# Kernel tuning notes

Measured on AMD Instinct MI355X. Metric: run time of the kernel, lower is better.

The kernel has to match this reference:

```python
import jax, jax.numpy as jnp
import numpy as np

B, T, C = 4, 2048, 768
H, KVH, D = 6, 6, 128
HALF = D // 2


def setup_inputs() -> dict:
    key = jax.random.key(0)
    ks = jax.random.split(key, 5)
    x = jax.random.normal(ks[0], (B, T, C), dtype=jnp.float32)
    # true rotary frequencies
    inv_freq = 1.0 / (10000.0 ** (jnp.arange(HALF, dtype=jnp.float32) / HALF))
    ang = jnp.arange(T, dtype=jnp.float32)[:, None] * inv_freq[None, :]  # [T, HALF]
    cos, sin = jnp.cos(ang), jnp.sin(ang)
    s = 0.02
    wq = jax.random.normal(ks[1], (H * D, C), dtype=jnp.float32) * s
    wk = jax.random.normal(ks[2], (KVH * D, C), dtype=jnp.float32) * s
    wv = jax.random.normal(ks[3], (KVH * D, C), dtype=jnp.float32) * s
    wproj = jax.random.normal(ks[4], (C, C), dtype=jnp.float32) * s
    return {"x": x, "cos": cos, "sin": sin, "wq": wq, "wk": wk, "wv": wv, "wproj": wproj}


def _norm(t, eps=1e-6):
    # torch: (x - mean) / (std + eps), std unbiased (ddof=1)
    mean = jnp.mean(t, axis=-1, keepdims=True)
    var = jnp.sum((t - mean) ** 2, axis=-1, keepdims=True) / (t.shape[-1] - 1)
    return (t - mean) / (jnp.sqrt(var) + eps)


def _rope(t, cos, sin):
    # t: [B, T, heads, D]; cos/sin: [T, HALF]
    x1, x2 = t[..., :HALF], t[..., HALF:]
    c = cos[None, :, None, :]
    s = sin[None, :, None, :]
    return jnp.concatenate([x1 * c + x2 * s, -x1 * s + x2 * c], axis=-1)


def reference(x, cos, sin, wq, wk, wv, wproj):
    q = jnp.einsum('btc,oc->bto', x, wq).reshape(B, T, H, D)
    k = jnp.einsum('btc,oc->bto', x, wk).reshape(B, T, KVH, D)
    v = jnp.einsum('btc,oc->bto', x, wv).reshape(B, T, KVH, D)
    q = _norm(_rope(q, cos, sin))
    k = _norm(_rope(k, cos, sin))
    # -> [B, heads, T, D]
    q = q.transpose(0, 2, 1, 3)
    k = k.transpose(0, 2, 1, 3)
    v = v.transpose(0, 2, 1, 3)
    # nrep = H // KVH == 1, repeat_kv is a no-op here
    scale = 1.0 / jnp.sqrt(jnp.float32(D))
    scores = jnp.einsum('bhtd,bhsd->bhts', q, k) * scale  # [B,H,T,T]
    causal = jnp.tril(jnp.ones((T, T), dtype=bool))
    scores = jnp.where(causal[None, None], scores, jnp.float32(-1e30))
    attn = jax.nn.softmax(scores, axis=-1)
    y = jnp.einsum('bhts,bhsd->bhtd', attn, v)
    y = y.transpose(0, 2, 1, 3).reshape(B, T, H * D)
    return jnp.einsum('bto,co->btc', y, wproj)
```

## Files before the change

### kernel.cpp

```cpp
#include <hip/hip_runtime.h>

#define BB 4
#define TT 2048
#define CC 768
#define HH 6
#define DD 128
#define BT (BB * TT)
#define HALF 64
#define QKSCALE 0.12753785627919282f

typedef __bf16 v8bf __attribute__((ext_vector_type(8)));
typedef float f32x4 __attribute__((ext_vector_type(4)));

__device__ __forceinline__ unsigned short f2b(float f) {
  union { float f; unsigned u; } v; v.f = f;
  unsigned r = v.u + 0x7FFFu + ((v.u >> 16) & 1u);
  return (unsigned short)(r >> 16);
}

__device__ __forceinline__ void load_lds16(const void* g, void* l) {
  __builtin_amdgcn_global_load_lds(
      (const __attribute__((address_space(1))) unsigned int*)g,
      (__attribute__((address_space(3))) unsigned int*)(unsigned int)(unsigned long long)(l),
      16, 0, 0);
}

__global__ __launch_bounds__(256) void cvt_f2b_kernel(const float* __restrict__ src,
                                                      unsigned short* __restrict__ dst,
                                                      int n4) {
  int i = blockIdx.x * 256 + threadIdx.x;
  if (i >= n4) return;
  float4 f = ((const float4*)src)[i];
  ushort4 o;
  o.x = f2b(f.x); o.y = f2b(f.y); o.z = f2b(f.z); o.w = f2b(f.w);
  ((ushort4*)dst)[i] = o;
}

__global__ __launch_bounds__(256) void cvt_w4_kernel(const float* __restrict__ w0,
                                                     const float* __restrict__ w1,
                                                     const float* __restrict__ w2,
                                                     const float* __restrict__ w3,
                                                     unsigned short* __restrict__ dst) {
  int bsel = blockIdx.x / 576;
  int i = (blockIdx.x % 576) * 256 + threadIdx.x;
  const float* src = bsel == 0 ? w0 : bsel == 1 ? w1 : bsel == 2 ? w2 : w3;
  float4 f = ((const float4*)src)[i];
  ushort4 o;
  o.x = f2b(f.x); o.y = f2b(f.y); o.z = f2b(f.z); o.w = f2b(f.w);
  ((ushort4*)(dst + bsel * 589824))[i] = o;
}

__global__ __launch_bounds__(256) void gemm_qkv(const unsigned short* __restrict__ A,
                                                const unsigned short* __restrict__ Wall,
                                                float* __restrict__ qout,
                                                float* __restrict__ kout,
                                                unsigned short* __restrict__ vt) {
  __shared__ __align__(16) unsigned short As[2][512 * 8];
  __shared__ __align__(16) unsigned short Bs[2][512 * 8];
  const int m0 = blockIdx.x * 128;
  const int wsel = blockIdx.y / HH, h = blockIdx.y % HH;
  const unsigned short* W = Wall + (size_t)wsel * 589824 + (size_t)h * 128 * CC;
  const int tid = threadIdx.x;
  const int wave = tid >> 6, lane = tid & 63;
  const int fr = lane & 15, quad = lane >> 4;
  const int wm = (wave & 1) * 64, wn = (wave >> 1) * 64;

  f32x4 acc[4][4];
#pragma unroll
  for (int i = 0; i < 4; i++)
#pragma unroll
    for (int j = 0; j < 4; j++) acc[i][j] = (f32x4){0.f, 0.f, 0.f, 0.f};

  auto stage = [&](int kk, int buf) {
#pragma unroll
    for (int it = 0; it < 2; it++) {
      int base_slot = wave * 128 + it * 64;
      int sigma = base_slot + lane;
      int r = sigma >> 2, g = (sigma & 3) ^ ((r >> 1) & 3);
      load_lds16(A + (size_t)(m0 + r) * CC + kk + g * 8, &As[buf][base_slot * 8]);
      load_lds16(W + (size_t)r * CC + kk + g * 8, &Bs[buf][base_slot * 8]);
    }
  };

  stage(0, 0);
  __syncthreads();
  for (int step = 0; step < CC / 32; step++) {
    int buf = step & 1;
    if (step + 1 < CC / 32) stage((step + 1) * 32, buf ^ 1);
    v8bf af[4], bfr[4];
#pragma unroll
    for (int i = 0; i < 4; i++) {
      int ra = wm + i * 16 + fr;
      af[i] = *(const v8bf*)&As[buf][(4 * ra + (quad ^ ((ra >> 1) & 3))) * 8];
      int rb = wn + i * 16 + fr;
      bfr[i] = *(const v8bf*)&Bs[buf][(4 * rb + (quad ^ ((rb >> 1) & 3))) * 8];
    }
#pragma unroll
    for (int i = 0; i < 4; i++)
#pragma unroll
      for (int j = 0; j < 4; j++)
        acc[i][j] = __builtin_amdgcn_mfma_f32_16x16x32_bf16(af[i], bfr[j], acc[i][j], 0, 0, 0);
    __syncthreads();
  }

  if (wsel < 2) {
    float* out = wsel ? kout : qout;
    const int orow = m0 + wm + quad * 4;
#pragma unroll
    for (int i = 0; i < 4; i++)
#pragma unroll
      for (int j = 0; j < 4; j++) {
        int oc = h * 128 + wn + j * 16 + fr;
#pragma unroll
        for (int r = 0; r < 4; r++)
          out[(size_t)(orow + i * 16 + r) * CC + oc] = acc[i][j][r];
      }
  } else {
#pragma unroll
    for (int i = 0; i < 4; i++) {
      int rr0 = m0 + wm + i * 16 + quad * 4;
      int b = rr0 >> 11, t0 = rr0 & 2047;
      int bh = b * HH + h;
#pragma unroll
      for (int j = 0; j < 4; j++) {
        int d = wn + j * 16 + fr;
        ushort4 u = { f2b(acc[i][j][0]), f2b(acc[i][j][1]),
                      f2b(acc[i][j][2]), f2b(acc[i][j][3]) };
        *(ushort4*)&vt[((size_t)bh * DD + d) * TT + t0] = u;
      }
    }
  }
}

__global__ __launch_bounds__(256) void gemm_w64(const unsigned short* __restrict__ A,
                                                const unsigned short* __restrict__ W,
                                                float* __restrict__ C) {
  __shared__ __align__(16) unsigned short As[2][256 * 8];
  __shared__ __align__(16) unsigned short Bs[2][512 * 8];
  const int m0 = blockIdx.x * 64, n0 = blockIdx.y * 128;
  const int tid = threadIdx.x;
  const int wave = tid >> 6, lane = tid & 63;
  const int fr = lane & 15, quad = lane >> 4;
  const int wm = (wave & 1) * 32, wn = (wave >> 1) * 64;

  f32x4 acc[2][4];
#pragma unroll
  for (int i = 0; i < 2; i++)
#pragma unroll
    for (int j = 0; j < 4; j++) acc[i][j] = (f32x4){0.f, 0.f, 0.f, 0.f};

  auto stage = [&](int kk, int buf) {
    {
      int base_slot = wave * 64;
      int sigma = base_slot + lane;
      int r = sigma >> 2, g = (sigma & 3) ^ ((r >> 1) & 3);
      load_lds16(A + (size_t)(m0 + r) * CC + kk + g * 8, &As[buf][base_slot * 8]);
    }
#pragma unroll
    for (int it = 0; it < 2; it++) {
      int base_slot = wave * 128 + it * 64;
      int sigma = base_slot + lane;
      int r = sigma >> 2, g = (sigma & 3) ^ ((r >> 1) & 3);
      load_lds16(W + (size_t)(n0 + r) * CC + kk + g * 8, &Bs[buf][base_slot * 8]);
    }
  };

  stage(0, 0);
  __syncthreads();
  for (int step = 0; step < CC / 32; step++) {
    int buf = step & 1;
    if (step + 1 < CC / 32) stage((step + 1) * 32, buf ^ 1);
    v8bf af[2], bfr[4];
#pragma unroll
    for (int i = 0; i < 2; i++) {
      int ra = wm + i * 16 + fr;
      af[i] = *(const v8bf*)&As[buf][(4 * ra + (quad ^ ((ra >> 1) & 3))) * 8];
    }
#pragma unroll
    for (int j = 0; j < 4; j++) {
      int rb = wn + j * 16 + fr;
      bfr[j] = *(const v8bf*)&Bs[buf][(4 * rb + (quad ^ ((rb >> 1) & 3))) * 8];
    }
#pragma unroll
    for (int i = 0; i < 2; i++)
#pragma unroll
      for (int j = 0; j < 4; j++)
        acc[i][j] = __builtin_amdgcn_mfma_f32_16x16x32_bf16(af[i], bfr[j], acc[i][j], 0, 0, 0);
    __syncthreads();
  }

  const int orow = m0 + wm + quad * 4;
#pragma unroll
  for (int i = 0; i < 2; i++)
#pragma unroll
    for (int j = 0; j < 4; j++) {
      int oc = n0 + wn + j * 16 + fr;
#pragma unroll
      for (int r = 0; r < 4; r++)
        C[(size_t)(orow + i * 16 + r) * CC + oc] = acc[i][j][r];
    }
}

__global__ __launch_bounds__(256) void rope_norm_kernel(const float* __restrict__ src,
                                                        unsigned short* __restrict__ dst,
                                                        const float* __restrict__ cosb,
                                                        const float* __restrict__ sinb) {
  int idx = blockIdx.x * 4 + (threadIdx.x >> 6);
  int lane = threadIdx.x & 63;
  int h = idx % HH;
  int bt = idx / HH;
  int tpos = bt & (TT - 1);
  int b = bt >> 11;
  size_t base = (size_t)bt * CC + h * DD;

  float x1 = src[base + lane];
  float x2 = src[base + HALF + lane];
  float c = cosb[tpos * HALF + lane];
  float s = sinb[tpos * HALF + lane];
  float o1 = x1 * c + x2 * s;
  float o2 = x2 * c - x1 * s;

  float sum = o1 + o2;
#pragma unroll
  for (int off = 32; off; off >>= 1) sum += __shfl_xor(sum, off);
  float mean = sum * (1.f / 128.f);
  float d1 = o1 - mean, d2 = o2 - mean;
  float vs = d1 * d1 + d2 * d2;
#pragma unroll
  for (int off = 32; off; off >>= 1) vs += __shfl_xor(vs, off);
  float inv = 1.f / (sqrtf(vs * (1.f / 127.f)) + 1e-6f);

  size_t obase = (((size_t)b * HH + h) * TT + tpos) * DD;
  dst[obase + lane] = f2b(d1 * inv);
  dst[obase + HALF + lane] = f2b(d2 * inv);
}

__global__ __launch_bounds__(128) void attn_mfma(const unsigned short* __restrict__ qtb,
                                                 const unsigned short* __restrict__ ktb,
                                                 const unsigned short* __restrict__ vtb,
                                                 float* __restrict__ Opart,
                                                 float* __restrict__ lpart) {
  __shared__ __align__(16) unsigned short Ks[2][512 * 8];
  __shared__ __align__(16) unsigned short Vts[2][512 * 8];
  __shared__ __align__(16) unsigned short Ps[2][32][40];

  const int u = blockIdx.x;
  const int qt = (TT / 64 - 1) - u / 48;
  const int r48 = u % 48;
  const int chunk = r48 / 24;
  const int bh = r48 % 24;
  const int tid = threadIdx.x;
  const int wave = tid >> 6, lane = tid & 63;
  const int fr = lane & 15, quad = lane >> 4;

  const size_t head_base = (size_t)bh * TT * DD;
  const int m0 = qt * 64 + wave * 32;
  const int jt0 = chunk ? (qt + 1) : 0;
  const int niter = qt + 1;

  v8bf qf[2][4];
#pragma unroll
  for (int qs = 0; qs < 2; qs++)
#pragma unroll
    for (int kb = 0; kb < 4; kb++)
      qf[qs][kb] = *(const v8bf*)(qtb + head_base +
                                  (size_t)(m0 + qs * 16 + fr) * DD + kb * 32 + quad * 8);

  f32x4 oacc[2][8];
#pragma unroll
  for (int qs = 0; qs < 2; qs++)
#pragma unroll
    for (int i = 0; i < 8; i++) oacc[qs][i] = (f32x4){0.f, 0.f, 0.f, 0.f};
  float lsum[2] = {0.f, 0.f};

  auto stage = [&](int jt, int buf) {
    const unsigned short* kbase = ktb + head_base + (size_t)(jt * 32) * DD;
    const unsigned short* vbase = vtb + head_base + jt * 32;
#pragma unroll
    for (int it = 0; it < 4; it++) {
      int base_slot = wave * 256 + it * 64;
      int sigma = base_slot + lane;
      int s = sigma >> 4, gk = (sigma & 15) ^ (s & 7);
      load_lds16(kbase + (size_t)s * DD + gk * 8, &Ks[buf][base_slot * 8]);
      int d = sigma >> 2, gv = (sigma & 3) ^ ((d >> 1) & 3);
      load_lds16(vbase + (size_t)d * TT + gv * 8, &Vts[buf][base_slot * 8]);
    }
  };

  stage(jt0, 0);
  __syncthreads();

  for (int it = 0; it < niter; it++) {
    const int jt = jt0 + it;
    const int buf = it & 1;
    if (it + 1 < niter) stage(jt + 1, buf ^ 1);

    if (jt * 32 <= m0 + 31) {
      const int j0 = jt * 32;
      f32x4 st[2][2];
#pragma unroll
      for (int qs = 0; qs < 2; qs++) { st[qs][0] = (f32x4){0,0,0,0}; st[qs][1] = (f32x4){0,0,0,0}; }
#pragma unroll
      for (int kb = 0; kb < 4; kb++) {
        int g = 4 * kb + quad;
        v8bf a0 = *(const v8bf*)&Ks[buf][(16 * fr + (g ^ (fr & 7))) * 8];
        v8bf a1 = *(const v8bf*)&Ks[buf][(16 * (fr + 16) + (g ^ (fr & 7))) * 8];
        st[0][0] = __builtin_amdgcn_mfma_f32_16x16x32_bf16(a0, qf[0][kb], st[0][0], 0, 0, 0);
        st[0][1] = __builtin_amdgcn_mfma_f32_16x16x32_bf16(a1, qf[0][kb], st[0][1], 0, 0, 0);
        st[1][0] = __builtin_amdgcn_mfma_f32_16x16x32_bf16(a0, qf[1][kb], st[1][0], 0, 0, 0);
        st[1][1] = __builtin_amdgcn_mfma_f32_16x16x32_bf16(a1, qf[1][kb], st[1][1], 0, 0, 0);
      }

#pragma unroll
      for (int qs = 0; qs < 2; qs++) {
        const int qrow = m0 + qs * 16 + fr;
        float p[8]; float ls = 0.f;
#pragma unroll
        for (int r = 0; r < 4; r++) {
          int c0 = j0 + quad * 4 + r;
          p[r]     = (c0      <= qrow) ? exp2f(st[qs][0][r] * QKSCALE) : 0.f;
          p[4 + r] = (c0 + 16 <= qrow) ? exp2f(st[qs][1][r] * QKSCALE) : 0.f;
          ls += p[r] + p[4 + r];
        }
        lsum[qs] += ls;
        ushort4 w0 = { f2b(p[0]), f2b(p[1]), f2b(p[2]), f2b(p[3]) };
        ushort4 w1 = { f2b(p[4]), f2b(p[5]), f2b(p[6]), f2b(p[7]) };
        *(ushort4*)&Ps[wave][qs * 16 + fr][quad * 4] = w0;
        *(ushort4*)&Ps[wave][qs * 16 + fr][16 + quad * 4] = w1;
      }

      v8bf pa0 = *(const v8bf*)&Ps[wave][fr][quad * 8];
      v8bf pa1 = *(const v8bf*)&Ps[wave][16 + fr][quad * 8];
#pragma unroll
      for (int nt2 = 0; nt2 < 8; nt2++) {
        int d = nt2 * 16 + fr;
        v8bf vb = *(const v8bf*)&Vts[buf][(4 * d + (quad ^ ((d >> 1) & 3))) * 8];
        oacc[0][nt2] = __builtin_amdgcn_mfma_f32_16x16x32_bf16(pa0, vb, oacc[0][nt2], 0, 0, 0);
        oacc[1][nt2] = __builtin_amdgcn_mfma_f32_16x16x32_bf16(pa1, vb, oacc[1][nt2], 0, 0, 0);
      }
    }
    __syncthreads();
  }

  float* Oc = Opart + (size_t)chunk * (BB * HH * TT * DD) + head_base;
#pragma unroll
  for (int qs = 0; qs < 2; qs++) {
    float l = lsum[qs];
    l += __shfl_xor(l, 16);
    l += __shfl_xor(l, 32);
    if (quad == 0)
      lpart[chunk * (BB * HH * TT) + bh * TT + m0 + qs * 16 + fr] = l;
#pragma unroll
    for (int nt2 = 0; nt2 < 8; nt2++)
#pragma unroll
      for (int r = 0; r < 4; r++)
        Oc[(size_t)(m0 + qs * 16 + quad * 4 + r) * DD + nt2 * 16 + fr] = oacc[qs][nt2][r];
  }
}

__global__ __launch_bounds__(256) void combine_kernel(const float* __restrict__ Opart,
                                                      const float* __restrict__ lpart,
                                                      unsigned short* __restrict__ yb) {
  int idx = blockIdx.x * 256 + threadIdx.x;
  int row = idx >> 5;
  int dg = (idx & 31) * 4;
  float4 o0 = *(const float4*)&Opart[(size_t)row * DD + dg];
  float4 o1 = *(const float4*)&Opart[(size_t)(BB * HH * TT) * DD + (size_t)row * DD + dg];
  float linv = 1.f / (lpart[row] + lpart[BB * HH * TT + row]);
  int bh = row >> 11, t = row & 2047;
  int b = bh / HH, h = bh % HH;
  ushort4 u = { f2b((o0.x + o1.x) * linv), f2b((o0.y + o1.y) * linv),
                f2b((o0.z + o1.z) * linv), f2b((o0.w + o1.w) * linv) };
  *(ushort4*)&yb[((size_t)(b * TT + t)) * CC + h * DD + dg] = u;
}

extern "C" void kernel_launch(void* const* d_in, const int* in_sizes, int n_in,
                              void* d_out, int out_size, void* d_ws, size_t ws_size,
                              hipStream_t stream) {
  const float* x     = (const float*)d_in[0];
  const float* cosb  = (const float*)d_in[1];
  const float* sinb  = (const float*)d_in[2];
  const float* wq    = (const float*)d_in[3];
  const float* wk    = (const float*)d_in[4];
  const float* wv    = (const float*)d_in[5];
  const float* wproj = (const float*)d_in[6];
  float* out = (float*)d_out;

  char* w = (char*)d_ws;
  float* q     = (float*)(w);
  float* kk    = (float*)(w + 25165824);
  float* Opart = (float*)(w);
  unsigned short* yb  = (unsigned short*)(w + 50331648);
  unsigned short* v_t = (unsigned short*)(w + 62914560);
  unsigned short* q_t = (unsigned short*)(w + 75497472);
  unsigned short* k_t = (unsigned short*)(w + 88080384);
  unsigned short* xb  = (unsigned short*)(w + 100663296);
  float* lpart        = (float*)(w + 100663296);
  unsigned short* wb  = (unsigned short*)(w + 113246208);

  const int nx4 = BT * CC / 4;

  cvt_f2b_kernel<<<nx4 / 256, 256, 0, stream>>>(x, xb, nx4);
  cvt_w4_kernel<<<2304, 256, 0, stream>>>(wq, wk, wv, wproj, wb);

  gemm_qkv<<<dim3(BT / 128, 3 * HH), 256, 0, stream>>>(xb, wb, q, kk, v_t);

  int nvec = BT * HH;
  rope_norm_kernel<<<nvec / 4, 256, 0, stream>>>(q, q_t, cosb, sinb);
  rope_norm_kernel<<<nvec / 4, 256, 0, stream>>>(kk, k_t, cosb, sinb);

  attn_mfma<<<1536, 128, 0, stream>>>(q_t, k_t, v_t, Opart, lpart);
  combine_kernel<<<6144, 256, 0, stream>>>(Opart, lpart, yb);

  gemm_w64<<<dim3(BT / 64, CC / 128), 256, 0, stream>>>(yb, wb + 3 * 589824, out);
}
```

Measured before the change: 245.4 us.

## Store Q/K as bf16 head-major, split attention into balanced KV chunks

The QKV GEMM now writes Q and K directly as bf16 in head-major layout, and rope/norm runs in place with the softmax scale folded into Q. This removes the fp32 round trip and the transposing write. The attention kernel is restructured into 4 waves of 16 query rows each, with a variable number of 16-tile KV chunks per query tile to balance causal work across 1920 blocks. It also skips the mask on full tiles, computes row sums with an MFMA against ones, and stores bf16 partial outputs. The combine kernel then sums a variable number of bf16 partials, which adds precision risk from bf16 partial accumulation and from the unbounded exp2 without a running max.

Result: no change. 246.8 us (+0.6%).

```diff
diff --git a/kernel.cpp b/kernel.cpp
--- a/kernel.cpp
+++ b/kernel.cpp
@@ -7,15 +7,30 @@
 #define DD 128
 #define BT (BB * TT)
 #define HALF 64
+#define NBH (BB * HH)
 #define QKSCALE 0.12753785627919282f
 
 typedef __bf16 v8bf __attribute__((ext_vector_type(8)));
 typedef float f32x4 __attribute__((ext_vector_type(4)));
+
+#if __has_builtin(__builtin_amdgcn_exp2f)
+#define EXP2(x) __builtin_amdgcn_exp2f(x)
+#else
+#define EXP2(x) exp2f(x)
+#endif
 
 __device__ __forceinline__ unsigned short f2b(float f) {
   union { float f; unsigned u; } v; v.f = f;
   unsigned r = v.u + 0x7FFFu + ((v.u >> 16) & 1u);
   return (unsigned short)(r >> 16);
+}
+__device__ __forceinline__ float b2f(unsigned short u) {
+  union { unsigned u; float f; } v; v.u = (unsigned)u << 16;
+  return v.f;
+}
+__device__ __forceinline__ unsigned pk2(float f0, float f1) {
+  union { float f; unsigned u; } a, b; a.f = f1; b.f = f0;
+  return __builtin_amdgcn_perm(a.u, b.u, 0x07060302u);
 }
 
 __device__ __forceinline__ void load_lds16(const void* g, void* l) {
@@ -52,8 +67,8 @@
 
 __global__ __launch_bounds__(256) void gemm_qkv(const unsigned short* __restrict__ A,
                                                 const unsigned short* __restrict__ Wall,
-                                                float* __restrict__ qout,
-                                                float* __restrict__ kout,
+                                                unsigned short* __restrict__ qb,
+                                                unsigned short* __restrict__ kb,
                                                 unsigned short* __restrict__ vt) {
   __shared__ __align__(16) unsigned short As[2][512 * 8];
   __shared__ __align__(16) unsigned short Bs[2][512 * 8];
@@ -104,17 +119,20 @@
   }
 
   if (wsel < 2) {
-    float* out = wsel ? kout : qout;
-    const int orow = m0 + wm + quad * 4;
-#pragma unroll
-    for (int i = 0; i < 4; i++)
+    unsigned short* dst = wsel ? kb : qb;
+#pragma unroll
+    for (int i = 0; i < 4; i++) {
+      int rr0 = m0 + wm + i * 16 + quad * 4;
+      int b = rr0 >> 11, t0 = rr0 & 2047;
+      size_t base = ((size_t)(b * HH + h) * TT + t0) * DD;
 #pragma unroll
       for (int j = 0; j < 4; j++) {
-        int oc = h * 128 + wn + j * 16 + fr;
+        int d = wn + j * 16 + fr;
 #pragma unroll
         for (int r = 0; r < 4; r++)
-          out[(size_t)(orow + i * 16 + r) * CC + oc] = acc[i][j][r];
+          dst[base + (size_t)r * DD + d] = f2b(acc[i][j][r]);
       }
+    }
   } else {
 #pragma unroll
     for (int i = 0; i < 4; i++) {
@@ -201,20 +219,17 @@
     }
 }
 
-__global__ __launch_bounds__(256) void rope_norm_kernel(const float* __restrict__ src,
-                                                        unsigned short* __restrict__ dst,
+__global__ __launch_bounds__(256) void rope_norm_kernel(unsigned short* __restrict__ qk,
                                                         const float* __restrict__ cosb,
-                                                        const float* __restrict__ sinb) {
+                                                        const float* __restrict__ sinb,
+                                                        float scale) {
   int idx = blockIdx.x * 4 + (threadIdx.x >> 6);
   int lane = threadIdx.x & 63;
-  int h = idx % HH;
-  int bt = idx / HH;
-  int tpos = bt & (TT - 1);
-  int b = bt >> 11;
-  size_t base = (size_t)bt * CC + h * DD;
-
-  float x1 = src[base + lane];
-  float x2 = src[base + HALF + lane];
+  int tpos = idx & (TT - 1);
+  size_t base = (size_t)idx * DD;
+
+  float x1 = b2f(qk[base + lane]);
+  float x2 = b2f(qk[base + HALF + lane]);
   float c = cosb[tpos * HALF + lane];
   float s = sinb[tpos * HALF + lane];
   float o1 = x1 * c + x2 * s;
@@ -228,57 +243,58 @@
   float vs = d1 * d1 + d2 * d2;
 #pragma unroll
   for (int off = 32; off; off >>= 1) vs += __shfl_xor(vs, off);
-  float inv = 1.f / (sqrtf(vs * (1.f / 127.f)) + 1e-6f);
-
-  size_t obase = (((size_t)b * HH + h) * TT + tpos) * DD;
-  dst[obase + lane] = f2b(d1 * inv);
-  dst[obase + HALF + lane] = f2b(d2 * inv);
-}
-
-__global__ __launch_bounds__(128) void attn_mfma(const unsigned short* __restrict__ qtb,
+  float inv = scale / (sqrtf(vs * (1.f / 127.f)) + 1e-6f);
+
+  qk[base + lane] = f2b(d1 * inv);
+  qk[base + HALF + lane] = f2b(d2 * inv);
+}
+
+__global__ __launch_bounds__(256) void attn_mfma(const unsigned short* __restrict__ qtb,
                                                  const unsigned short* __restrict__ ktb,
                                                  const unsigned short* __restrict__ vtb,
-                                                 float* __restrict__ Opart,
+                                                 unsigned short* __restrict__ Opart,
                                                  float* __restrict__ lpart) {
   __shared__ __align__(16) unsigned short Ks[2][512 * 8];
   __shared__ __align__(16) unsigned short Vts[2][512 * 8];
-  __shared__ __align__(16) unsigned short Ps[2][32][40];
+  __shared__ __align__(16) unsigned short Ps[4][16][40];
 
   const int u = blockIdx.x;
-  const int qt = (TT / 64 - 1) - u / 48;
-  const int r48 = u % 48;
-  const int chunk = r48 / 24;
-  const int bh = r48 % 24;
+  const int bh = u % NBH;
+  const int uu = u / NBH;
+  int qt, c;
+  if (uu < 32)      { qt = 31 - (uu >> 2);        c = uu & 3; }
+  else if (uu < 56) { int k = uu - 32; int q3 = k / 3; qt = 23 - q3; c = k - q3 * 3; }
+  else if (uu < 72) { int k = uu - 56; qt = 15 - (k >> 1); c = k & 1; }
+  else              { qt = 7 - (uu - 72);         c = 0; }
+  const int t0 = c * 16;
+  const int t1 = min(t0 + 16, 2 * qt + 2);
+  const int niter = t1 - t0;
+
   const int tid = threadIdx.x;
   const int wave = tid >> 6, lane = tid & 63;
   const int fr = lane & 15, quad = lane >> 4;
-
   const size_t head_base = (size_t)bh * TT * DD;
-  const int m0 = qt * 64 + wave * 32;
-  const int jt0 = chunk ? (qt + 1) : 0;
-  const int niter = qt + 1;
-
-  v8bf qf[2][4];
-#pragma unroll
-  for (int qs = 0; qs < 2; qs++)
-#pragma unroll
-    for (int kb = 0; kb < 4; kb++)
-      qf[qs][kb] = *(const v8bf*)(qtb + head_base +
-                                  (size_t)(m0 + qs * 16 + fr) * DD + kb * 32 + quad * 8);
-
-  f32x4 oacc[2][8];
-#pragma unroll
-  for (int qs = 0; qs < 2; qs++)
-#pragma unroll
-    for (int i = 0; i < 8; i++) oacc[qs][i] = (f32x4){0.f, 0.f, 0.f, 0.f};
-  float lsum[2] = {0.f, 0.f};
+  const int m0 = qt * 64 + wave * 16;
+
+  v8bf qf[4];
+#pragma unroll
+  for (int kbk = 0; kbk < 4; kbk++)
+    qf[kbk] = *(const v8bf*)(qtb + head_base + (size_t)(m0 + fr) * DD + kbk * 32 + quad * 8);
+
+  const __bf16 one_bf = (__bf16)1.0f;
+  v8bf ones = {one_bf, one_bf, one_bf, one_bf, one_bf, one_bf, one_bf, one_bf};
+
+  f32x4 oacc[8];
+#pragma unroll
+  for (int i = 0; i < 8; i++) oacc[i] = (f32x4){0.f, 0.f, 0.f, 0.f};
+  f32x4 lacc = (f32x4){0.f, 0.f, 0.f, 0.f};
 
   auto stage = [&](int jt, int buf) {
     const unsigned short* kbase = ktb + head_base + (size_t)(jt * 32) * DD;
     const unsigned short* vbase = vtb + head_base + jt * 32;
 #pragma unroll
-    for (int it = 0; it < 4; it++) {
-      int base_slot = wave * 256 + it * 64;
+    for (int it = 0; it < 2; it++) {
+      int base_slot = it * 256 + wave * 64;
       int sigma = base_slot + lane;
       int s = sigma >> 4, gk = (sigma & 15) ^ (s & 7);
       load_lds16(kbase + (size_t)s * DD + gk * 8, &Ks[buf][base_slot * 8]);
@@ -287,90 +303,89 @@
     }
   };
 
-  stage(jt0, 0);
+  stage(t0, 0);
   __syncthreads();
 
   for (int it = 0; it < niter; it++) {
-    const int jt = jt0 + it;
+    const int jt = t0 + it;
     const int buf = it & 1;
     if (it + 1 < niter) stage(jt + 1, buf ^ 1);
 
-    if (jt * 32 <= m0 + 31) {
-      const int j0 = jt * 32;
-      f32x4 st[2][2];
-#pragma unroll
-      for (int qs = 0; qs < 2; qs++) { st[qs][0] = (f32x4){0,0,0,0}; st[qs][1] = (f32x4){0,0,0,0}; }
-#pragma unroll
-      for (int kb = 0; kb < 4; kb++) {
-        int g = 4 * kb + quad;
+    const int j0 = jt * 32;
+    if (j0 <= m0 + 15) {
+      f32x4 st0 = (f32x4){0.f, 0.f, 0.f, 0.f}, st1 = (f32x4){0.f, 0.f, 0.f, 0.f};
+#pragma unroll
+      for (int kbk = 0; kbk < 4; kbk++) {
+        int g = 4 * kbk + quad;
         v8bf a0 = *(const v8bf*)&Ks[buf][(16 * fr + (g ^ (fr & 7))) * 8];
         v8bf a1 = *(const v8bf*)&Ks[buf][(16 * (fr + 16) + (g ^ (fr & 7))) * 8];
-        st[0][0] = __builtin_amdgcn_mfma_f32_16x16x32_bf16(a0, qf[0][kb], st[0][0], 0, 0, 0);
-        st[0][1] = __builtin_amdgcn_mfma_f32_16x16x32_bf16(a1, qf[0][kb], st[0][1], 0, 0, 0);
-        st[1][0] = __builtin_amdgcn_mfma_f32_16x16x32_bf16(a0, qf[1][kb], st[1][0], 0, 0, 0);
-        st[1][1] = __builtin_amdgcn_mfma_f32_16x16x32_bf16(a1, qf[1][kb], st[1][1], 0, 0, 0);
+        st0 = __builtin_amdgcn_mfma_f32_16x16x32_bf16(a0, qf[kbk], st0, 0, 0, 0);
+        st1 = __builtin_amdgcn_mfma_f32_16x16x32_bf16(a1, qf[kbk], st1, 0, 0, 0);
       }
 
-#pragma unroll
-      for (int qs = 0; qs < 2; qs++) {
-        const int qrow = m0 + qs * 16 + fr;
-        float p[8]; float ls = 0.f;
+      float p[8];
+      if (j0 + 31 > m0) {
+        const int qrow = m0 + fr;
 #pragma unroll
         for (int r = 0; r < 4; r++) {
           int c0 = j0 + quad * 4 + r;
-          p[r]     = (c0      <= qrow) ? exp2f(st[qs][0][r] * QKSCALE) : 0.f;
-          p[4 + r] = (c0 + 16 <= qrow) ? exp2f(st[qs][1][r] * QKSCALE) : 0.f;
-          ls += p[r] + p[4 + r];
+          p[r]     = (c0      <= qrow) ? EXP2(st0[r]) : 0.f;
+          p[4 + r] = (c0 + 16 <= qrow) ? EXP2(st1[r]) : 0.f;
         }
-        lsum[qs] += ls;
-        ushort4 w0 = { f2b(p[0]), f2b(p[1]), f2b(p[2]), f2b(p[3]) };
-        ushort4 w1 = { f2b(p[4]), f2b(p[5]), f2b(p[6]), f2b(p[7]) };
-        *(ushort4*)&Ps[wave][qs * 16 + fr][quad * 4] = w0;
-        *(ushort4*)&Ps[wave][qs * 16 + fr][16 + quad * 4] = w1;
+      } else {
+#pragma unroll
+        for (int r = 0; r < 4; r++) { p[r] = EXP2(st0[r]); p[4 + r] = EXP2(st1[r]); }
       }
-
-      v8bf pa0 = *(const v8bf*)&Ps[wave][fr][quad * 8];
-      v8bf pa1 = *(const v8bf*)&Ps[wave][16 + fr][quad * 8];
+      uint2 w0 = { pk2(p[0], p[1]), pk2(p[2], p[3]) };
+      uint2 w1 = { pk2(p[4], p[5]), pk2(p[6], p[7]) };
+      *(uint2*)&Ps[wave][fr][quad * 4] = w0;
+      *(uint2*)&Ps[wave][fr][16 + quad * 4] = w1;
+
+      v8bf pa = *(const v8bf*)&Ps[wave][fr][quad * 8];
 #pragma unroll
       for (int nt2 = 0; nt2 < 8; nt2++) {
         int d = nt2 * 16 + fr;
         v8bf vb = *(const v8bf*)&Vts[buf][(4 * d + (quad ^ ((d >> 1) & 3))) * 8];
-        oacc[0][nt2] = __builtin_amdgcn_mfma_f32_16x16x32_bf16(pa0, vb, oacc[0][nt2], 0, 0, 0);
-        oacc[1][nt2] = __builtin_amdgcn_mfma_f32_16x16x32_bf16(pa1, vb, oacc[1][nt2], 0, 0, 0);
+        oacc[nt2] = __builtin_amdgcn_mfma_f32_16x16x32_bf16(pa, vb, oacc[nt2], 0, 0, 0);
       }
+      lacc = __builtin_amdgcn_mfma_f32_16x16x32_bf16(pa, ones, lacc, 0, 0, 0);
     }
     __syncthreads();
   }
 
-  float* Oc = Opart + (size_t)chunk * (BB * HH * TT * DD) + head_base;
-#pragma unroll
-  for (int qs = 0; qs < 2; qs++) {
-    float l = lsum[qs];
-    l += __shfl_xor(l, 16);
-    l += __shfl_xor(l, 32);
-    if (quad == 0)
-      lpart[chunk * (BB * HH * TT) + bh * TT + m0 + qs * 16 + fr] = l;
-#pragma unroll
-    for (int nt2 = 0; nt2 < 8; nt2++)
-#pragma unroll
-      for (int r = 0; r < 4; r++)
-        Oc[(size_t)(m0 + qs * 16 + quad * 4 + r) * DD + nt2 * 16 + fr] = oacc[qs][nt2][r];
-  }
-}
-
-__global__ __launch_bounds__(256) void combine_kernel(const float* __restrict__ Opart,
+  unsigned short* Oc = Opart + (size_t)c * (NBH * TT * DD) + head_base;
+#pragma unroll
+  for (int nt2 = 0; nt2 < 8; nt2++)
+#pragma unroll
+    for (int r = 0; r < 4; r++)
+      Oc[(size_t)(m0 + quad * 4 + r) * DD + nt2 * 16 + fr] = f2b(oacc[nt2][r]);
+  if (fr == 0) {
+#pragma unroll
+    for (int r = 0; r < 4; r++)
+      lpart[c * (NBH * TT) + bh * TT + m0 + quad * 4 + r] = lacc[r];
+  }
+}
+
+__global__ __launch_bounds__(256) void combine_kernel(const unsigned short* __restrict__ Opart,
                                                       const float* __restrict__ lpart,
                                                       unsigned short* __restrict__ yb) {
   int idx = blockIdx.x * 256 + threadIdx.x;
   int row = idx >> 5;
   int dg = (idx & 31) * 4;
-  float4 o0 = *(const float4*)&Opart[(size_t)row * DD + dg];
-  float4 o1 = *(const float4*)&Opart[(size_t)(BB * HH * TT) * DD + (size_t)row * DD + dg];
-  float linv = 1.f / (lpart[row] + lpart[BB * HH * TT + row]);
-  int bh = row >> 11, t = row & 2047;
+  int t = row & 2047;
+  int qt = t >> 6;
+  int nc = (2 * qt + 2 + 15) >> 4;
+
+  float a0 = 0.f, a1 = 0.f, a2 = 0.f, a3 = 0.f, l = 0.f;
+  for (int cchunk = 0; cchunk < nc; cchunk++) {
+    ushort4 o = *(const ushort4*)&Opart[(size_t)cchunk * (NBH * TT * DD) + (size_t)row * DD + dg];
+    a0 += b2f(o.x); a1 += b2f(o.y); a2 += b2f(o.z); a3 += b2f(o.w);
+    l += lpart[cchunk * (NBH * TT) + row];
+  }
+  float linv = 1.f / l;
+  int bh = row >> 11;
   int b = bh / HH, h = bh % HH;
-  ushort4 u = { f2b((o0.x + o1.x) * linv), f2b((o0.y + o1.y) * linv),
-                f2b((o0.z + o1.z) * linv), f2b((o0.w + o1.w) * linv) };
+  ushort4 u = { f2b(a0 * linv), f2b(a1 * linv), f2b(a2 * linv), f2b(a3 * linv) };
   *(ushort4*)&yb[((size_t)(b * TT + t)) * CC + h * DD + dg] = u;
 }
 
@@ -387,29 +402,27 @@
   float* out = (float*)d_out;
 
   char* w = (char*)d_ws;
-  float* q     = (float*)(w);
-  float* kk    = (float*)(w + 25165824);
-  float* Opart = (float*)(w);
-  unsigned short* yb  = (unsigned short*)(w + 50331648);
-  unsigned short* v_t = (unsigned short*)(w + 62914560);
-  unsigned short* q_t = (unsigned short*)(w + 75497472);
-  unsigned short* k_t = (unsigned short*)(w + 88080384);
-  unsigned short* xb  = (unsigned short*)(w + 100663296);
-  float* lpart        = (float*)(w + 100663296);
-  unsigned short* wb  = (unsigned short*)(w + 113246208);
+  unsigned short* q_t   = (unsigned short*)(w);
+  unsigned short* k_t   = (unsigned short*)(w + 12582912);
+  unsigned short* v_t   = (unsigned short*)(w + 25165824);
+  unsigned short* yb    = (unsigned short*)(w + 37748736);
+  unsigned short* xb    = (unsigned short*)(w + 50331648);
+  float*          lpart = (float*)(w + 50331648);
+  unsigned short* wb    = (unsigned short*)(w + 62914560);
+  unsigned short* Opart = (unsigned short*)(w + 67633152);
 
   const int nx4 = BT * CC / 4;
 
   cvt_f2b_kernel<<<nx4 / 256, 256, 0, stream>>>(x, xb, nx4);
   cvt_w4_kernel<<<2304, 256, 0, stream>>>(wq, wk, wv, wproj, wb);
 
-  gemm_qkv<<<dim3(BT / 128, 3 * HH), 256, 0, stream>>>(xb, wb, q, kk, v_t);
-
-  int nvec = BT * HH;
-  rope_norm_kernel<<<nvec / 4, 256, 0, stream>>>(q, q_t, cosb, sinb);
-  rope_norm_kernel<<<nvec / 4, 256, 0, stream>>>(kk, k_t, cosb, sinb);
-
-  attn_mfma<<<1536, 128, 0, stream>>>(q_t, k_t, v_t, Opart, lpart);
+  gemm_qkv<<<dim3(BT / 128, 3 * HH), 256, 0, stream>>>(xb, wb, q_t, k_t, v_t);
+
+  int nvec = NBH * TT;
+  rope_norm_kernel<<<nvec / 4, 256, 0, stream>>>(q_t, cosb, sinb, QKSCALE);
+  rope_norm_kernel<<<nvec / 4, 256, 0, stream>>>(k_t, cosb, sinb, 1.0f);
+
+  attn_mfma<<<1920, 256, 0, stream>>>(q_t, k_t, v_t, Opart, lpart);
   combine_kernel<<<6144, 256, 0, stream>>>(Opart, lpart, yb);
 
   gemm_w64<<<dim3(BT / 64, CC / 128), 256, 0, stream>>>(yb, wb + 3 * 589824, out);
```
